# Kernel tuning notes

Hardware: AMD Instinct MI355X
Metric: run time of the kernel (lower is better)

Reference implementation:

```python
import jax, jax.numpy as jnp
import numpy as np
import math

D_MODEL = 512
N_HEADS = 8
D_K = D_MODEL // N_HEADS
B, N = 2, 2048


def setup_inputs() -> dict:
    key = jax.random.key(0)
    ks = jax.random.split(key, 13)
    s = 1.0 / math.sqrt(D_MODEL)
    inp = {
        "x": jax.random.normal(ks[0], (B, N, D_MODEL), dtype=jnp.float32),
        "D": jax.random.uniform(ks[1], (B, N, N), dtype=jnp.float32),
        "A": jax.random.uniform(ks[2], (B, N, N), dtype=jnp.float32),
        "Wq": jax.random.normal(ks[3], (D_MODEL, D_MODEL), dtype=jnp.float32) * s,
        "bq": jnp.zeros((D_MODEL,), dtype=jnp.float32),
        "Wk": jax.random.normal(ks[4], (D_MODEL, D_MODEL), dtype=jnp.float32) * s,
        "bk": jnp.zeros((D_MODEL,), dtype=jnp.float32),
        "Wv": jax.random.normal(ks[5], (D_MODEL, D_MODEL), dtype=jnp.float32) * s,
        "bv": jnp.zeros((D_MODEL,), dtype=jnp.float32),
        "Wo": jax.random.normal(ks[6], (D_MODEL, D_MODEL), dtype=jnp.float32) * s,
        "bo": jnp.zeros((D_MODEL,), dtype=jnp.float32),
        # learned per-head bias scalars; init nonzero so biases matter numerically
        "w_d": jax.random.normal(ks[7], (1, N_HEADS, 1, 1), dtype=jnp.float32) * 0.1,
        "w_a": jax.random.normal(ks[8], (1, N_HEADS, 1, 1), dtype=jnp.float32) * 0.1,
    }
    return inp


def reference(x, D, A, Wq, bq, Wk, bk, Wv, bv, Wo, bo, w_d, w_a):
    b, n, _ = x.shape
    # project and split heads: (B, H, N, d_k)
    def heads(W, bias):
        return (x @ W.T + bias).reshape(b, n, N_HEADS, D_K).transpose(0, 2, 1, 3)
    q = heads(Wq, bq)
    k = heads(Wk, bk)
    v = heads(Wv, bv)
    scale = 1.0 / math.sqrt(D_K)
    # (B, H, N, N) scores with learned-scalar-weighted tree biases
    scores = jnp.einsum("bhqd,bhkd->bhqk", q, k) * scale
    scores = scores + w_d * D[:, None, :, :] + w_a * A[:, None, :, :]
    attn = jax.nn.softmax(scores, axis=-1)
    out = jnp.einsum("bhqk,bhkd->bhqd", attn, v)
    out = out.transpose(0, 2, 1, 3).reshape(b, n, D_MODEL)
    return out @ Wo.T + bo
```

## Files before the change

### kernel.cpp

```cpp
#include <hip/hip_runtime.h>
#include <hip/hip_bf16.h>
#include <math.h>

typedef unsigned short ushort_t;
typedef unsigned int   uint_t;
typedef __attribute__((ext_vector_type(8))) short  bf16x8;
typedef __attribute__((ext_vector_type(4))) float  f32x4;
typedef __attribute__((ext_vector_type(4))) int    int4v;
typedef __attribute__((ext_vector_type(2))) int    i32x2;
typedef __attribute__((ext_vector_type(4))) short  s16x4;

#define MFMA16(a, b, c) __builtin_amdgcn_mfma_f32_16x16x32_bf16((a), (b), (c), 0, 0, 0)

static constexpr int BATCH = 2;
static constexpr int SEQ   = 2048;
static constexpr int DMODEL = 512;
static constexpr int NHEADS = 8;
static constexpr int DK    = 64;
static constexpr int MROWS = BATCH * SEQ;
static constexpr int XE = MROWS * DMODEL;
static constexpr int WE = DMODEL * DMODEL;
static constexpr int NQKV = 3 * DMODEL;
static constexpr int NSPLIT = 4;
static constexpr int KB_PER = (SEQ / 64) / NSPLIT;

static constexpr float QSCALE_L2E = 0.18033688011112043f;
static constexpr float L2E = 1.4426950408889634f;

__device__ __forceinline__ ushort_t f2bf(float f) {
  unsigned int u = __builtin_bit_cast(unsigned int, f);
  u = (u + 0x7FFFu + ((u >> 16) & 1u)) >> 16;
  return (ushort_t)u;
}

__device__ __forceinline__ float fexp2(float x) {
  float r;
  asm("v_exp_f32 %0, %1" : "=v"(r) : "v"(x));
  return r;
}

__device__ __forceinline__ int cvt_pk_bf16(float a, float b) {
  int r;
  asm("v_cvt_pk_bf16_f32 %0, %1, %2" : "=v"(r) : "v"(a), "v"(b));
  return r;
}

__device__ __forceinline__ float rowmax16(float x) {
  int t;
  t = __builtin_amdgcn_mov_dpp(__builtin_bit_cast(int, x), 0xB1, 0xF, 0xF, true);
  x = fmaxf(x, __builtin_bit_cast(float, t));
  t = __builtin_amdgcn_mov_dpp(__builtin_bit_cast(int, x), 0x4E, 0xF, 0xF, true);
  x = fmaxf(x, __builtin_bit_cast(float, t));
  t = __builtin_amdgcn_mov_dpp(__builtin_bit_cast(int, x), 0x141, 0xF, 0xF, true);
  x = fmaxf(x, __builtin_bit_cast(float, t));
  t = __builtin_amdgcn_mov_dpp(__builtin_bit_cast(int, x), 0x140, 0xF, 0xF, true);
  x = fmaxf(x, __builtin_bit_cast(float, t));
  return x;
}

__device__ __forceinline__ void async16(const ushort_t* g, ushort_t* l) {
  __builtin_amdgcn_global_load_lds(
      (const __attribute__((address_space(1))) unsigned int*)g,
      (__attribute__((address_space(3))) unsigned int*)l, 16, 0, 0);
}

__global__ __launch_bounds__(256) void convert_kernel(
    const float* __restrict__ x,  const float* __restrict__ wq,
    const float* __restrict__ wk, const float* __restrict__ wv,
    const float* __restrict__ wo,
    const float* __restrict__ bq, const float* __restrict__ bk,
    const float* __restrict__ bv,
    ushort_t* __restrict__ dst, float* __restrict__ bqkv) {
  const int bid = blockIdx.x;
  if (bid == (XE + 4 * WE) / 1024) {
    for (int i = threadIdx.x; i < NQKV; i += 256) {
      bqkv[i] = (i < 512) ? bq[i] * QSCALE_L2E
              : (i < 1024) ? bk[i - 512] : bv[i - 1024];
    }
    return;
  }
  int e = (bid * 256 + threadIdx.x) * 4;
  const float* src;
  int off;
  float qs = 1.0f;
  if (e < XE)                { src = x;  off = e; }
  else if (e < XE + WE)      { src = wq; off = e - XE; qs = QSCALE_L2E; }
  else if (e < XE + 2 * WE)  { src = wk; off = e - XE - WE; }
  else if (e < XE + 3 * WE)  { src = wv; off = e - XE - 2 * WE; }
  else                       { src = wo; off = e - XE - 3 * WE; }
  float4 f = *reinterpret_cast<const float4*>(&src[off]);
  s16x4 v;
  v[0] = (short)f2bf(f.x * qs); v[1] = (short)f2bf(f.y * qs);
  v[2] = (short)f2bf(f.z * qs); v[3] = (short)f2bf(f.w * qs);
  *reinterpret_cast<s16x4*>(&dst[e]) = v;
}

__global__ __launch_bounds__(256) void pack_da_kernel(
    const float* __restrict__ Dm, const float* __restrict__ Am,
    uint_t* __restrict__ out) {
  int e = (blockIdx.x * 256 + threadIdx.x) * 4;
  float4 d = *reinterpret_cast<const float4*>(&Dm[e]);
  float4 a = *reinterpret_cast<const float4*>(&Am[e]);
  int4v v;
  v[0] = (int)((uint_t)f2bf(d.x) | ((uint_t)f2bf(a.x) << 16));
  v[1] = (int)((uint_t)f2bf(d.y) | ((uint_t)f2bf(a.y) << 16));
  v[2] = (int)((uint_t)f2bf(d.z) | ((uint_t)f2bf(a.z) << 16));
  v[3] = (int)((uint_t)f2bf(d.w) | ((uint_t)f2bf(a.w) << 16));
  *reinterpret_cast<int4v*>(&out[e]) = v;
}

template <bool F32OUT>
__global__ __launch_bounds__(256) void gemm_bt(
    const ushort_t* __restrict__ A, const ushort_t* __restrict__ Bt,
    const float* __restrict__ bias, void* __restrict__ C,
    int N, int K) {
  __shared__ ushort_t As[64][64];
  __shared__ ushort_t Bs[64][64];
  const int tid  = threadIdx.x;
  const int wave = tid >> 6, lane = tid & 63;
  const int quad = lane >> 4, l15 = lane & 15;
  const int m0 = blockIdx.y * 64, n0 = blockIdx.x * 64;

  f32x4 acc[4] = {};

  const int lrow = lane >> 3, slot = lane & 7;
  const int cswz = 8 * (slot ^ lrow);
  const ushort_t* ag = A  + (size_t)(m0 + wave * 16 + lrow) * K + cswz;
  const ushort_t* bg = Bt + (size_t)(n0 + wave * 16 + lrow) * K + cswz;
  ushort_t* la0 = &As[wave * 16][0];
  ushort_t* la1 = &As[wave * 16 + 8][0];
  ushort_t* lb0 = &Bs[wave * 16][0];
  ushort_t* lb1 = &Bs[wave * 16 + 8][0];

  const int swz = l15 & 7;

  for (int k0 = 0; k0 < K; k0 += 64) {
    __syncthreads();
    async16(ag + k0, la0);
    async16(ag + k0 + 8 * (size_t)K, la1);
    async16(bg + k0, lb0);
    async16(bg + k0 + 8 * (size_t)K, lb1);
    asm volatile("s_waitcnt vmcnt(0)" ::: "memory");
    __syncthreads();
#pragma unroll
    for (int s = 0; s < 2; s++) {
      const int acol = 8 * ((s * 4 + quad) ^ swz);
      bf16x8 af = *reinterpret_cast<const bf16x8*>(&As[wave * 16 + l15][acol]);
#pragma unroll
      for (int t = 0; t < 4; t++) {
        bf16x8 bfr = *reinterpret_cast<const bf16x8*>(&Bs[t * 16 + l15][acol]);
        acc[t] = MFMA16(af, bfr, acc[t]);
      }
    }
  }

#pragma unroll
  for (int t = 0; t < 4; t++) {
    const int col = n0 + t * 16 + l15;
    const float bv = bias[col];
#pragma unroll
    for (int rr = 0; rr < 4; rr++) {
      const int row = m0 + wave * 16 + quad * 4 + rr;
      const float v = acc[t][rr] + bv;
      if (F32OUT) reinterpret_cast<float*>(C)[(size_t)row * N + col] = v;
      else        reinterpret_cast<ushort_t*>(C)[(size_t)row * N + col] = f2bf(v);
    }
  }
}

__global__ __launch_bounds__(256) void attn_kernel(
    const ushort_t* __restrict__ QKV, const uint_t* __restrict__ DA,
    const float* __restrict__ wd, const float* __restrict__ wa,
    float* __restrict__ Opart, float* __restrict__ Mp, float* __restrict__ Lp) {
  const int qb = blockIdx.x, h = blockIdx.y;
  const int b = blockIdx.z / NSPLIT, split = blockIdx.z % NSPLIT;
  const int tid = threadIdx.x;
  const int wave = tid >> 6, lane = tid & 63;
  const int quad = lane >> 4, l15 = lane & 15;
  const int q0 = qb * 64;
  const float wdh = wd[h] * L2E, wah = wa[h] * L2E;

  __shared__ ushort_t Ks[64][64];
  __shared__ ushort_t Vts[64][64];
  __shared__ __align__(16) ushort_t Ps[4][16][72];

  const int qrow = q0 + wave * 16 + l15;
  bf16x8 qf[2];
#pragma unroll
  for (int s = 0; s < 2; s++)
    qf[s] = *reinterpret_cast<const bf16x8*>(
        &QKV[(size_t)(b * SEQ + qrow) * NQKV + h * DK + s * 32 + quad * 8]);

  bf16x8 ones;
#pragma unroll
  for (int j = 0; j < 8; j++) ones[j] = (short)0x3F80;

  float m_run[4], l_run[4];
  f32x4 o[4] = {};
#pragma unroll
  for (int rr = 0; rr < 4; rr++) { m_run[rr] = -INFINITY; l_run[rr] = 0.f; }

  const int lrow = lane >> 3, slot = lane & 7;
  const ushort_t* kg = QKV + (size_t)(b * SEQ + wave * 16 + lrow) * NQKV +
                       512 + h * DK + 8 * (slot ^ lrow);
  ushort_t* lk0 = &Ks[wave * 16][0];
  ushort_t* lk1 = &Ks[wave * 16 + 8][0];

  const int u  = tid >> 3;
  const int c7 = tid & 7;
  const int sc = c7 * 8;
  const int kv = ((u & 3) << 4) | (u >> 2);
  const ushort_t* vg = QKV + (size_t)(b * SEQ + kv) * NQKV + 1024 + h * DK + sc;
  const int col0 = (u & 7) + 8 * ((u >> 3) ^ c7);
  const int col1 = (u & 7) + 8 * (((u >> 3) + 4) ^ c7);

  const int swz = l15 & 7;

  const uint_t* dap[4];
#pragma unroll
  for (int rr = 0; rr < 4; rr++)
    dap[rr] = DA + (size_t)b * SEQ * SEQ +
              (size_t)(q0 + wave * 16 + quad * 4 + rr) * SEQ + l15;

  for (int kbi = 0; kbi < KB_PER; kbi++) {
    const int k0 = (split * KB_PER + kbi) * 64;
    __syncthreads();
    async16(kg + (size_t)k0 * NQKV, lk0);
    async16(kg + (size_t)(k0 + 8) * NQKV, lk1);
    bf16x8 v0 = *reinterpret_cast<const bf16x8*>(vg + (size_t)k0 * NQKV);
    bf16x8 v1 = *reinterpret_cast<const bf16x8*>(vg + (size_t)(k0 + 8) * NQKV);
#pragma unroll
    for (int j = 0; j < 8; j++) {
      Vts[sc + j][col0] = (ushort_t)v0[j];
      Vts[sc + j][col1] = (ushort_t)v1[j];
    }
    asm volatile("s_waitcnt vmcnt(0)" ::: "memory");
    __syncthreads();

    uint_t da[4][4];
#pragma unroll
    for (int t = 0; t < 4; t++) {
#pragma unroll
      for (int rr = 0; rr < 4; rr++) da[t][rr] = dap[rr][k0 + t * 16];
    }

    f32x4 sacc[4];
#pragma unroll
    for (int t = 0; t < 4; t++) {
      bf16x8 kf0 = *reinterpret_cast<const bf16x8*>(&Ks[t * 16 + l15][8 * (quad ^ swz)]);
      bf16x8 kf1 = *reinterpret_cast<const bf16x8*>(&Ks[t * 16 + l15][8 * ((4 + quad) ^ swz)]);
      f32x4 z = {};
      z = MFMA16(qf[0], kf0, z);
      sacc[t] = MFMA16(qf[1], kf1, z);
    }

    float sv[4][4];
    float mx[4] = {-INFINITY, -INFINITY, -INFINITY, -INFINITY};
#pragma unroll
    for (int t = 0; t < 4; t++) {
#pragma unroll
      for (int rr = 0; rr < 4; rr++) {
        const float fd = __builtin_bit_cast(float, da[t][rr] << 16);
        const float fa = __builtin_bit_cast(float, da[t][rr] & 0xFFFF0000u);
        float s = fmaf(wdh, fd, fmaf(wah, fa, sacc[t][rr]));
        sv[t][rr] = s;
        mx[rr] = fmaxf(mx[rr], s);
      }
    }
#pragma unroll
    for (int rr = 0; rr < 4; rr++) mx[rr] = rowmax16(mx[rr]);

    bool grow = false;
#pragma unroll
    for (int rr = 0; rr < 4; rr++) grow |= (mx[rr] > m_run[rr] + 11.5f);
    if (__ballot(grow)) {
      float alpha[4];
#pragma unroll
      for (int rr = 0; rr < 4; rr++) {
        const float mn = fmaxf(m_run[rr], mx[rr]);
        alpha[rr] = fexp2(m_run[rr] - mn);
        m_run[rr] = mn;
        l_run[rr] *= alpha[rr];
      }
#pragma unroll
      for (int dt = 0; dt < 4; dt++)
#pragma unroll
        for (int rr = 0; rr < 4; rr++) o[dt][rr] *= alpha[rr];
    }

#pragma unroll
    for (int rr = 0; rr < 4; rr++) {
      const float m = m_run[rr];
      i32x2 w;
      w[0] = cvt_pk_bf16(fexp2(sv[0][rr] - m), fexp2(sv[1][rr] - m));
      w[1] = cvt_pk_bf16(fexp2(sv[2][rr] - m), fexp2(sv[3][rr] - m));
      *reinterpret_cast<i32x2*>(&Ps[wave][quad * 4 + rr][l15 * 4]) = w;
    }

    asm volatile("s_waitcnt lgkmcnt(0)" ::: "memory");

    f32x4 rsacc = {};
#pragma unroll
    for (int s2 = 0; s2 < 2; s2++) {
      bf16x8 pf = *reinterpret_cast<const bf16x8*>(&Ps[wave][l15][s2 * 32 + quad * 8]);
#pragma unroll
      for (int dt = 0; dt < 4; dt++) {
        const int vrow = dt * 16 + l15;
        const int vcb = (s2 * 4 + quad) ^ (vrow >> 3);
        bf16x8 vf = *reinterpret_cast<const bf16x8*>(&Vts[vrow][vcb * 8]);
        o[dt] = MFMA16(pf, vf, o[dt]);
      }
      rsacc = MFMA16(pf, ones, rsacc);
    }
#pragma unroll
    for (int rr = 0; rr < 4; rr++) l_run[rr] += rsacc[rr];
  }

  const int pidx = (((b * NHEADS + h) * 32 + qb) * NSPLIT + split);
  float* op = Opart + (size_t)pidx * 4096;
#pragma unroll
  for (int dt = 0; dt < 4; dt++) {
#pragma unroll
    for (int rr = 0; rr < 4; rr++) {
      const int row = wave * 16 + quad * 4 + rr;
      op[row * 64 + dt * 16 + l15] = o[dt][rr];
    }
  }
  if (l15 == 0) {
#pragma unroll
    for (int rr = 0; rr < 4; rr++) {
      const int row = wave * 16 + quad * 4 + rr;
      Mp[(size_t)pidx * 64 + row] = m_run[rr];
      Lp[(size_t)pidx * 64 + row] = l_run[rr];
    }
  }
}

__global__ __launch_bounds__(256) void combine_kernel(
    const float* __restrict__ Opart, const float* __restrict__ Mp,
    const float* __restrict__ Lp, ushort_t* __restrict__ AO) {
  const int qb = blockIdx.x, h = blockIdx.y, b = blockIdx.z;
  const int tid = threadIdx.x;
  const int lane = tid & 63, wq = tid >> 6;
  const int pidx0 = ((b * NHEADS + h) * 32 + qb) * NSPLIT;

  for (int r = 0; r < 16; r++) {
    const int q = wq * 16 + r;
    float m[NSPLIT], l[NSPLIT];
    float M = -INFINITY;
#pragma unroll
    for (int s = 0; s < NSPLIT; s++) {
      m[s] = Mp[(size_t)(pidx0 + s) * 64 + q];
      l[s] = Lp[(size_t)(pidx0 + s) * 64 + q];
      M = fmaxf(M, m[s]);
    }
    float L = 0.f, acc = 0.f;
#pragma unroll
    for (int s = 0; s < NSPLIT; s++) {
      const float w = fexp2(m[s] - M);
      L += l[s] * w;
      acc += Opart[(size_t)(pidx0 + s) * 4096 + q * 64 + lane] * w;
    }
    const int row = b * SEQ + qb * 64 + q;
    AO[(size_t)row * DMODEL + h * DK + lane] = f2bf(acc / L);
  }
}

extern "C" void kernel_launch(void* const* d_in, const int* in_sizes, int n_in,
                              void* d_out, int out_size, void* d_ws, size_t ws_size,
                              hipStream_t stream) {
  const float* x  = (const float*)d_in[0];
  const float* Dm = (const float*)d_in[1];
  const float* Am = (const float*)d_in[2];
  const float* Wq = (const float*)d_in[3];
  const float* bq = (const float*)d_in[4];
  const float* Wk = (const float*)d_in[5];
  const float* bk = (const float*)d_in[6];
  const float* Wv = (const float*)d_in[7];
  const float* bv = (const float*)d_in[8];
  const float* Wo = (const float*)d_in[9];
  const float* bo = (const float*)d_in[10];
  const float* wd = (const float*)d_in[11];
  const float* wa = (const float*)d_in[12];

  char* ws = (char*)d_ws;
  size_t off = 0;
  ushort_t* xb    = (ushort_t*)(ws + off); off += (size_t)XE * 2;
  ushort_t* wqkvb = (ushort_t*)(ws + off); off += (size_t)3 * WE * 2;
  ushort_t* wob   = (ushort_t*)(ws + off); off += (size_t)WE * 2;
  ushort_t* QKVb  = (ushort_t*)(ws + off); off += (size_t)MROWS * NQKV * 2;
  ushort_t* AO    = (ushort_t*)(ws + off); off += (size_t)XE * 2;
  float*    bqkv  = (float*)(ws + off);    off += (size_t)NQKV * 4;
  off = (off + 255) & ~(size_t)255;
  uint_t*   DAb   = (uint_t*)(ws + off);   off += (size_t)BATCH * SEQ * SEQ * 4;
  float*    Opart = (float*)(ws + off);    off += (size_t)512 * NSPLIT * 4096 * 4;
  float*    Mpart = (float*)(ws + off);    off += (size_t)512 * NSPLIT * 64 * 4;
  float*    Lpart = (float*)(ws + off);

  const int conv_blocks = (XE + 4 * WE) / 1024;
  convert_kernel<<<conv_blocks + 1, 256, 0, stream>>>(
      x, Wq, Wk, Wv, Wo, bq, bk, bv, xb, bqkv);
  pack_da_kernel<<<(BATCH * SEQ * SEQ) / 1024, 256, 0, stream>>>(Dm, Am, DAb);

  dim3 qkvgrid(NQKV / 64, MROWS / 64);
  gemm_bt<false><<<qkvgrid, 256, 0, stream>>>(xb, wqkvb, bqkv, QKVb, NQKV, DMODEL);

  dim3 agrid(SEQ / 64, NHEADS, BATCH * NSPLIT);
  attn_kernel<<<agrid, 256, 0, stream>>>(QKVb, DAb, wd, wa, Opart, Mpart, Lpart);
  dim3 cgrid(SEQ / 64, NHEADS, BATCH);
  combine_kernel<<<cgrid, 256, 0, stream>>>(Opart, Mpart, Lpart, AO);

  dim3 ogrid(DMODEL / 64, MROWS / 64);
  gemm_bt<true><<<ogrid, 256, 0, stream>>>(AO, wob, bo, (float*)d_out, DMODEL, DMODEL);
}
```

Before: 226.9 us.

## Merge convert and DA-pack kernels, enlarge GEMM tiles to 128x64

Folds the D/A packing kernel into the weight/activation conversion kernel so a single launch does both. Both projection GEMMs now use a 128x64 tile with a 2x2 wave layout, giving each wave a 64x32 sub-tile and more MFMA work per LDS fragment load. The attention kernel computes DA addresses inline instead of keeping per-row pointers, which lowers register pressure but adds address arithmetic. The larger tiles halve the GEMM block count, which may underfill the GPU for the small output GEMM.

```diff
diff --git a/kernel.cpp b/kernel.cpp
--- a/kernel.cpp
+++ b/kernel.cpp
@@ -64,19 +64,36 @@
       (__attribute__((address_space(3))) unsigned int*)l, 16, 0, 0);
 }
 
-__global__ __launch_bounds__(256) void convert_kernel(
+static constexpr int CONV_BLOCKS = (XE + 4 * WE) / 1024;
+static constexpr int PACK_BLOCKS = (BATCH * SEQ * SEQ) / 1024;
+
+__global__ __launch_bounds__(256) void convert_pack_kernel(
     const float* __restrict__ x,  const float* __restrict__ wq,
     const float* __restrict__ wk, const float* __restrict__ wv,
     const float* __restrict__ wo,
     const float* __restrict__ bq, const float* __restrict__ bk,
     const float* __restrict__ bv,
-    ushort_t* __restrict__ dst, float* __restrict__ bqkv) {
+    const float* __restrict__ Dm, const float* __restrict__ Am,
+    ushort_t* __restrict__ dst, float* __restrict__ bqkv,
+    uint_t* __restrict__ DAb) {
   const int bid = blockIdx.x;
-  if (bid == (XE + 4 * WE) / 1024) {
+  if (bid == CONV_BLOCKS) {
     for (int i = threadIdx.x; i < NQKV; i += 256) {
       bqkv[i] = (i < 512) ? bq[i] * QSCALE_L2E
               : (i < 1024) ? bk[i - 512] : bv[i - 1024];
     }
+    return;
+  }
+  if (bid > CONV_BLOCKS) {
+    int e = ((bid - CONV_BLOCKS - 1) * 256 + threadIdx.x) * 4;
+    float4 d = *reinterpret_cast<const float4*>(&Dm[e]);
+    float4 a = *reinterpret_cast<const float4*>(&Am[e]);
+    int4v v;
+    v[0] = (int)((uint_t)f2bf(d.x) | ((uint_t)f2bf(a.x) << 16));
+    v[1] = (int)((uint_t)f2bf(d.y) | ((uint_t)f2bf(a.y) << 16));
+    v[2] = (int)((uint_t)f2bf(d.z) | ((uint_t)f2bf(a.z) << 16));
+    v[3] = (int)((uint_t)f2bf(d.w) | ((uint_t)f2bf(a.w) << 16));
+    *reinterpret_cast<int4v*>(&DAb[e]) = v;
     return;
   }
   int e = (bid * 256 + threadIdx.x) * 4;
@@ -95,40 +112,28 @@
   *reinterpret_cast<s16x4*>(&dst[e]) = v;
 }
 
-__global__ __launch_bounds__(256) void pack_da_kernel(
-    const float* __restrict__ Dm, const float* __restrict__ Am,
-    uint_t* __restrict__ out) {
-  int e = (blockIdx.x * 256 + threadIdx.x) * 4;
-  float4 d = *reinterpret_cast<const float4*>(&Dm[e]);
-  float4 a = *reinterpret_cast<const float4*>(&Am[e]);
-  int4v v;
-  v[0] = (int)((uint_t)f2bf(d.x) | ((uint_t)f2bf(a.x) << 16));
-  v[1] = (int)((uint_t)f2bf(d.y) | ((uint_t)f2bf(a.y) << 16));
-  v[2] = (int)((uint_t)f2bf(d.z) | ((uint_t)f2bf(a.z) << 16));
-  v[3] = (int)((uint_t)f2bf(d.w) | ((uint_t)f2bf(a.w) << 16));
-  *reinterpret_cast<int4v*>(&out[e]) = v;
-}
-
 template <bool F32OUT>
-__global__ __launch_bounds__(256) void gemm_bt(
+__global__ __launch_bounds__(256) void gemm_bt128x64(
     const ushort_t* __restrict__ A, const ushort_t* __restrict__ Bt,
     const float* __restrict__ bias, void* __restrict__ C,
     int N, int K) {
-  __shared__ ushort_t As[64][64];
+  __shared__ ushort_t As[128][64];
   __shared__ ushort_t Bs[64][64];
   const int tid  = threadIdx.x;
   const int wave = tid >> 6, lane = tid & 63;
   const int quad = lane >> 4, l15 = lane & 15;
-  const int m0 = blockIdx.y * 64, n0 = blockIdx.x * 64;
-
-  f32x4 acc[4] = {};
+  const int m0 = blockIdx.y * 128, n0 = blockIdx.x * 64;
+  const int wr = (wave >> 1) * 64, wc = (wave & 1) * 32;
+
+  f32x4 acc[4][2] = {};
 
   const int lrow = lane >> 3, slot = lane & 7;
   const int cswz = 8 * (slot ^ lrow);
-  const ushort_t* ag = A  + (size_t)(m0 + wave * 16 + lrow) * K + cswz;
+  const ushort_t* ag = A  + (size_t)(m0 + wave * 8 + lrow) * K + cswz;
   const ushort_t* bg = Bt + (size_t)(n0 + wave * 16 + lrow) * K + cswz;
-  ushort_t* la0 = &As[wave * 16][0];
-  ushort_t* la1 = &As[wave * 16 + 8][0];
+  ushort_t* la[4];
+#pragma unroll
+  for (int r0 = 0; r0 < 4; r0++) la[r0] = &As[r0 * 32 + wave * 8][0];
   ushort_t* lb0 = &Bs[wave * 16][0];
   ushort_t* lb1 = &Bs[wave * 16 + 8][0];
 
@@ -136,8 +141,9 @@
 
   for (int k0 = 0; k0 < K; k0 += 64) {
     __syncthreads();
-    async16(ag + k0, la0);
-    async16(ag + k0 + 8 * (size_t)K, la1);
+#pragma unroll
+    for (int r0 = 0; r0 < 4; r0++)
+      async16(ag + k0 + (size_t)(r0 * 32) * K, la[r0]);
     async16(bg + k0, lb0);
     async16(bg + k0 + 8 * (size_t)K, lb1);
     asm volatile("s_waitcnt vmcnt(0)" ::: "memory");
@@ -145,25 +151,34 @@
 #pragma unroll
     for (int s = 0; s < 2; s++) {
       const int acol = 8 * ((s * 4 + quad) ^ swz);
-      bf16x8 af = *reinterpret_cast<const bf16x8*>(&As[wave * 16 + l15][acol]);
-#pragma unroll
-      for (int t = 0; t < 4; t++) {
-        bf16x8 bfr = *reinterpret_cast<const bf16x8*>(&Bs[t * 16 + l15][acol]);
-        acc[t] = MFMA16(af, bfr, acc[t]);
+      bf16x8 af[4], bfr[2];
+#pragma unroll
+      for (int i = 0; i < 4; i++)
+        af[i] = *reinterpret_cast<const bf16x8*>(&As[wr + i * 16 + l15][acol]);
+#pragma unroll
+      for (int j = 0; j < 2; j++)
+        bfr[j] = *reinterpret_cast<const bf16x8*>(&Bs[wc + j * 16 + l15][acol]);
+#pragma unroll
+      for (int i = 0; i < 4; i++)
+#pragma unroll
+        for (int j = 0; j < 2; j++)
+          acc[i][j] = MFMA16(af[i], bfr[j], acc[i][j]);
+    }
+  }
+
+#pragma unroll
+  for (int j = 0; j < 2; j++) {
+    const int col = n0 + wc + j * 16 + l15;
+    const float bv = bias[col];
+#pragma unroll
+    for (int i = 0; i < 4; i++) {
+#pragma unroll
+      for (int rr = 0; rr < 4; rr++) {
+        const int row = m0 + wr + i * 16 + quad * 4 + rr;
+        const float v = acc[i][j][rr] + bv;
+        if (F32OUT) reinterpret_cast<float*>(C)[(size_t)row * N + col] = v;
+        else        reinterpret_cast<ushort_t*>(C)[(size_t)row * N + col] = f2bf(v);
       }
-    }
-  }
-
-#pragma unroll
-  for (int t = 0; t < 4; t++) {
-    const int col = n0 + t * 16 + l15;
-    const float bv = bias[col];
-#pragma unroll
-    for (int rr = 0; rr < 4; rr++) {
-      const int row = m0 + wave * 16 + quad * 4 + rr;
-      const float v = acc[t][rr] + bv;
-      if (F32OUT) reinterpret_cast<float*>(C)[(size_t)row * N + col] = v;
-      else        reinterpret_cast<ushort_t*>(C)[(size_t)row * N + col] = f2bf(v);
     }
   }
 }
@@ -215,12 +230,7 @@
   const int col1 = (u & 7) + 8 * (((u >> 3) + 4) ^ c7);
 
   const int swz = l15 & 7;
-
-  const uint_t* dap[4];
-#pragma unroll
-  for (int rr = 0; rr < 4; rr++)
-    dap[rr] = DA + (size_t)b * SEQ * SEQ +
-              (size_t)(q0 + wave * 16 + quad * 4 + rr) * SEQ + l15;
+  const uint_t* DArow = DA + (size_t)b * SEQ * SEQ;
 
   for (int kbi = 0; kbi < KB_PER; kbi++) {
     const int k0 = (split * KB_PER + kbi) * 64;
@@ -240,8 +250,12 @@
     uint_t da[4][4];
 #pragma unroll
     for (int t = 0; t < 4; t++) {
-#pragma unroll
-      for (int rr = 0; rr < 4; rr++) da[t][rr] = dap[rr][k0 + t * 16];
+      const int kk = k0 + t * 16 + l15;
+#pragma unroll
+      for (int rr = 0; rr < 4; rr++) {
+        const int qg = q0 + wave * 16 + quad * 4 + rr;
+        da[t][rr] = DArow[(size_t)qg * SEQ + kk];
+      }
     }
 
     f32x4 sacc[4];
@@ -397,19 +411,17 @@
   float*    Mpart = (float*)(ws + off);    off += (size_t)512 * NSPLIT * 64 * 4;
   float*    Lpart = (float*)(ws + off);
 
-  const int conv_blocks = (XE + 4 * WE) / 1024;
-  convert_kernel<<<conv_blocks + 1, 256, 0, stream>>>(
-      x, Wq, Wk, Wv, Wo, bq, bk, bv, xb, bqkv);
-  pack_da_kernel<<<(BATCH * SEQ * SEQ) / 1024, 256, 0, stream>>>(Dm, Am, DAb);
-
-  dim3 qkvgrid(NQKV / 64, MROWS / 64);
-  gemm_bt<false><<<qkvgrid, 256, 0, stream>>>(xb, wqkvb, bqkv, QKVb, NQKV, DMODEL);
+  convert_pack_kernel<<<CONV_BLOCKS + 1 + PACK_BLOCKS, 256, 0, stream>>>(
+      x, Wq, Wk, Wv, Wo, bq, bk, bv, Dm, Am, xb, bqkv, DAb);
+
+  dim3 qkvgrid(NQKV / 64, MROWS / 128);
+  gemm_bt128x64<false><<<qkvgrid, 256, 0, stream>>>(xb, wqkvb, bqkv, QKVb, NQKV, DMODEL);
 
   dim3 agrid(SEQ / 64, NHEADS, BATCH * NSPLIT);
   attn_kernel<<<agrid, 256, 0, stream>>>(QKVb, DAb, wd, wa, Opart, Mpart, Lpart);
   dim3 cgrid(SEQ / 64, NHEADS, BATCH);
   combine_kernel<<<cgrid, 256, 0, stream>>>(Opart, Mpart, Lpart, AO);
 
-  dim3 ogrid(DMODEL / 64, MROWS / 64);
-  gemm_bt<true><<<ogrid, 256, 0, stream>>>(AO, wob, bo, (float*)d_out, DMODEL, DMODEL);
-}
+  dim3 ogrid(DMODEL / 64, MROWS / 128);
+  gemm_bt128x64<true><<<ogrid, 256, 0, stream>>>(AO, wob, bo, (float*)d_out, DMODEL, DMODEL);
+}
```

Measured after the change: 217.8 us. 4.0% less time.
